# Performance work log

Hardware: AMD Instinct MI355X
Metric: run time of the kernel (lower is better)

The kernel has to match this reference:

```python
import jax, jax.numpy as jnp
import numpy as np

NUM_EXPERTS = 8
TOP_K = 2
D = 512
F = 2048
B, L = 4, 1024


def setup_inputs() -> dict:
    key = jax.random.key(0)
    ks = jax.random.split(key, 5)
    std = D ** -0.5
    return {
        "x": jax.random.normal(ks[0], (B, L, D), jnp.float32),
        "gate_w": jax.random.normal(ks[1], (NUM_EXPERTS, D), jnp.float32) * std,
        "w1": jax.random.normal(ks[2], (NUM_EXPERTS, F, D), jnp.float32) * std,
        "w2": jax.random.normal(ks[3], (NUM_EXPERTS, D, F), jnp.float32) * (F ** -0.5),
        "w3": jax.random.normal(ks[4], (NUM_EXPERTS, F, D), jnp.float32) * std,
    }


def reference(x, gate_w, w1, w2, w3):
    b, l, d = x.shape
    xf = x.reshape(-1, d)                      # [T, D]
    T = xf.shape[0]
    router_logits = xf @ gate_w.T              # [T, E]
    # top-k routing in float32 (as in original), softmax over selected logits
    topk_w, topk_idx = jax.lax.top_k(router_logits.astype(jnp.float32), TOP_K)
    topk_w = jax.nn.softmax(topk_w, axis=-1).astype(x.dtype)  # [T, K]
    # combine weights per (token, expert): scatter top-k weights into dense [T, E]
    cw = jnp.zeros((T, NUM_EXPERTS), x.dtype)
    cw = cw.at[jnp.arange(T)[:, None], topk_idx].add(topk_w)
    # per-expert gated FFN (SiLU(x w1^T) * (x w3^T)) w2^T, batched over experts
    h = jax.nn.silu(jnp.einsum('td,efd->etf', xf, w1)) * jnp.einsum('td,efd->etf', xf, w3)
    y = jnp.einsum('etf,edf->etd', h, w2)      # [E, T, D]
    out = jnp.einsum('te,etd->td', cw, y)      # weighted combine
    return out.reshape(b, l, d), router_logits
```

## Files before the change

### kernel.cpp

```cpp
#include <hip/hip_runtime.h>

#define TTOK 4096
#define NEXP 8
#define DDIM 512
#define FDIM 2048

typedef __attribute__((ext_vector_type(8))) short short8;
typedef __attribute__((ext_vector_type(4))) float floatx4;

__device__ __forceinline__ ushort f2b(float f) {
  unsigned u = __float_as_uint(f);
  u += 0x7fffu + ((u >> 16) & 1u);
  return (ushort)(u >> 16);
}

__device__ __forceinline__ void load16(void* lds, const void* g) {
  __builtin_amdgcn_global_load_lds(
      (const __attribute__((address_space(1))) unsigned int*)g,
      (__attribute__((address_space(3))) unsigned int*)lds, 16, 0, 0);
}

__global__ __launch_bounds__(256) void k_cvt3(
    const float* __restrict__ s1, ushort* __restrict__ d1,
    const float* __restrict__ s2, ushort* __restrict__ d2,
    const float* __restrict__ s3, ushort* __restrict__ d3, int n4)
{
  int i = blockIdx.x * 256 + threadIdx.x;
  const float* s; ushort* d; int j;
  if (i < n4)            { s = s1; d = d1; j = i; }
  else if (i < 2 * n4)   { s = s2; d = d2; j = i - n4; }
  else                   { s = s3; d = d3; j = i - 2 * n4; }
  float4 v = ((const float4*)s)[j];
  ushort4 b = { f2b(v.x), f2b(v.y), f2b(v.z), f2b(v.w) };
  ((ushort4*)d)[j] = b;
}

__global__ __launch_bounds__(256) void k_logits(
    const float* __restrict__ x, const float* __restrict__ gw,
    float* __restrict__ logits, int* __restrict__ tok_e,
    float2* __restrict__ tok_w, ushort* __restrict__ xb)
{
  const int lane = threadIdx.x & 63;
  const int t = blockIdx.x * 4 + (threadIdx.x >> 6);
  float xv[8];
#pragma unroll
  for (int i = 0; i < 8; ++i) xv[i] = x[(size_t)t * DDIM + lane + 64 * i];
#pragma unroll
  for (int i = 0; i < 8; ++i) xb[(size_t)t * DDIM + lane + 64 * i] = f2b(xv[i]);
  float lg[8];
#pragma unroll
  for (int e = 0; e < 8; ++e) {
    float a = 0.f;
#pragma unroll
    for (int i = 0; i < 8; ++i) a += xv[i] * gw[e * DDIM + lane + 64 * i];
#pragma unroll
    for (int s = 32; s; s >>= 1) a += __shfl_xor(a, s, 64);
    lg[e] = a;
  }
  if (lane < 8) logits[(size_t)t * 8 + lane] = lg[lane];
  if (lane == 0) {
    int i0 = 0; float v0 = lg[0];
#pragma unroll
    for (int e = 1; e < 8; ++e) { if (lg[e] > v0) { v0 = lg[e]; i0 = e; } }
    int i1 = -1; float v1 = -3.4e38f;
#pragma unroll
    for (int e = 0; e < 8; ++e) { if (e != i0 && lg[e] > v1) { v1 = lg[e]; i1 = e; } }
    float ex = expf(v1 - v0);
    float inv = 1.f / (1.f + ex);
    tok_e[t] = i0 | (i1 << 4);
    tok_w[t] = make_float2(inv, ex * inv);
  }
}

__global__ __launch_bounds__(256) void k_build(
    const int* __restrict__ tok_e, const float2* __restrict__ tok_w,
    int* __restrict__ counts, int* __restrict__ lists, float* __restrict__ wts)
{
  const int e = blockIdx.x;
  const int tid = threadIdx.x;
  const int lane = tid & 63, wid = tid >> 6;
  __shared__ int wcnt[4];
  __shared__ int sbase;
  if (tid == 0) sbase = 0;
  __syncthreads();

  for (int c = 0; c < TTOK; c += 256) {
    int t = c + tid;
    int pe = tok_e[t];
    bool m0 = (pe & 15) == e;
    bool m1 = ((pe >> 4) & 15) == e;
    bool m = m0 || m1;
    unsigned long long b = __ballot(m);
    int lpre = __popcll(b & ((1ull << lane) - 1ull));
    if (lane == 0) wcnt[wid] = __popcll(b);
    __syncthreads();
    int woff = 0;
#pragma unroll
    for (int i = 0; i < 4; ++i) if (i < wid) woff += wcnt[i];
    if (m) {
      float2 w = tok_w[t];
      int pos = sbase + woff + lpre;
      lists[e * TTOK + pos] = t;
      wts[e * TTOK + pos] = m0 ? w.x : w.y;
    }
    __syncthreads();
    if (tid == 0) sbase += wcnt[0] + wcnt[1] + wcnt[2] + wcnt[3];
    __syncthreads();
  }
  if (tid == 0) counts[e] = sbase;
}

__global__ void k_offsets(const int* __restrict__ counts, int* __restrict__ offs) {
  if (threadIdx.x == 0 && blockIdx.x == 0) {
    int s = 0;
    for (int e = 0; e < NEXP; ++e) { offs[e] = s; s += counts[e]; }
  }
}

__global__ __launch_bounds__(512) void k_ffn1(
    const ushort* __restrict__ xb, const ushort* __restrict__ w1b,
    const ushort* __restrict__ w3b, const int* __restrict__ counts,
    const int* __restrict__ offs, const int* __restrict__ lists,
    ushort* __restrict__ H)
{
  const int bid = blockIdx.x;
  const int widx = (bid & 7) * 512 + (bid >> 3);
  const int mt = widx & 31, e = (widx >> 5) & 7, f0t = widx >> 8;
  const int ne = counts[e];
  const int m0 = mt * 128;
  if (m0 >= ne) return;
  const int f0 = f0t * 128;
  const int tid = threadIdx.x;

  __shared__ ushort xs[2][128][32];
  __shared__ ushort w1s[2][128][32];
  __shared__ ushort w3s[2][128][32];
  __shared__ int toks[128];

  if (tid < 128) {
    int p = m0 + tid;
    toks[tid] = (p < ne) ? lists[e * TTOK + p] : 0;
  }
  __syncthreads();

  const int wid = tid >> 6, lane = tid & 63;
  const int wm = wid >> 2, wn = wid & 3;
  const int lr = lane & 15, lgp = lane >> 4;

  const int sr = tid >> 2, sc = (tid & 3) << 3;
  const ushort* xS  = xb + (size_t)toks[sr] * DDIM + sc;
  const ushort* w1S = w1b + (size_t)e * FDIM * DDIM + (size_t)(f0 + sr) * DDIM + sc;
  const ushort* w3S = w3b + (size_t)e * FDIM * DDIM + (size_t)(f0 + sr) * DDIM + sc;

#define FFN1_STAGE(B)                                                      \
  {                                                                        \
    load16((char*)&xs[B][0][0] + wid * 1024, xS);                          \
    load16((char*)&w1s[B][0][0] + wid * 1024, w1S);                        \
    load16((char*)&w3s[B][0][0] + wid * 1024, w3S);                        \
    xS += 32; w1S += 32; w3S += 32;                                        \
  }

#define FFN1_COMPUTE(B)                                                    \
  {                                                                        \
    short8 af[4], f1[2], f3[2];                                            \
    _Pragma("unroll")                                                      \
    for (int mf = 0; mf < 4; ++mf)                                         \
      af[mf] = *(const short8*)&xs[B][wm * 64 + mf * 16 + lr][lgp * 8];    \
    _Pragma("unroll")                                                      \
    for (int nf = 0; nf < 2; ++nf) {                                       \
      f1[nf] = *(const short8*)&w1s[B][wn * 32 + nf * 16 + lr][lgp * 8];   \
      f3[nf] = *(const short8*)&w3s[B][wn * 32 + nf * 16 + lr][lgp * 8];   \
    }                                                                      \
    _Pragma("unroll")                                                      \
    for (int mf = 0; mf < 4; ++mf)                                         \
      _Pragma("unroll")                                                    \
      for (int nf = 0; nf < 2; ++nf) {                                     \
        acc1[mf][nf] = __builtin_amdgcn_mfma_f32_16x16x32_bf16(            \
            af[mf], f1[nf], acc1[mf][nf], 0, 0, 0);                        \
        acc3[mf][nf] = __builtin_amdgcn_mfma_f32_16x16x32_bf16(            \
            af[mf], f3[nf], acc3[mf][nf], 0, 0, 0);                        \
      }                                                                    \
  }

  floatx4 acc1[4][2], acc3[4][2];
#pragma unroll
  for (int a = 0; a < 4; ++a)
#pragma unroll
    for (int b = 0; b < 2; ++b) { acc1[a][b] = (floatx4)0.f; acc3[a][b] = (floatx4)0.f; }

  FFN1_STAGE(0);
  __syncthreads();

  for (int t = 0; t < 16; t += 2) {
    if (t + 1 < 16) FFN1_STAGE(1);
    FFN1_COMPUTE(0);
    __syncthreads();
    if (t + 2 < 16) FFN1_STAGE(0);
    FFN1_COMPUTE(1);
    __syncthreads();
  }

  const int hb = offs[e];
#pragma unroll
  for (int mf = 0; mf < 4; ++mf) {
#pragma unroll
    for (int j = 0; j < 4; ++j) {
      int rloc = wm * 64 + mf * 16 + lgp * 4 + j;
      int p = m0 + rloc;
      if (p < ne) {
#pragma unroll
        for (int nf = 0; nf < 2; ++nf) {
          float h1 = acc1[mf][nf][j];
          float h3 = acc3[mf][nf][j];
          float sig = 1.f / (1.f + __expf(-h1));
          int f = f0 + wn * 32 + nf * 16 + lr;
          H[(size_t)(hb + p) * FDIM + f] = f2b(h1 * sig * h3);
        }
      }
    }
  }
#undef FFN1_STAGE
#undef FFN1_COMPUTE
}

__global__ __launch_bounds__(512) void k_ffn2(
    const ushort* __restrict__ w2b, const int* __restrict__ counts,
    const int* __restrict__ offs, const int* __restrict__ lists,
    const float* __restrict__ wts, const ushort* __restrict__ H,
    float* __restrict__ out)
{
  const int bid = blockIdx.x;
  const int widx = (bid & 7) * 128 + (bid >> 3);
  const int mt = widx & 31, e = (widx >> 5) & 7, d0t = widx >> 8;
  const int ne = counts[e];
  const int m0 = mt * 128;
  if (m0 >= ne) return;
  const int d0 = d0t * 128;
  const int tid = threadIdx.x;

  __shared__ ushort hs[2][2][128][32];
  __shared__ ushort w2s[2][2][128][32];
  __shared__ int toks[128];
  __shared__ float twt[128];

  const int hb = offs[e];
  if (tid < 128) {
    int p = m0 + tid;
    bool v = p < ne;
    toks[tid] = v ? lists[e * TTOK + p] : 0;
    twt[tid] = v ? wts[e * TTOK + p] : 0.f;
  }

  const int wid = tid >> 6, lane = tid & 63;
  const int wm = wid >> 2, wn = wid & 3;
  const int lr = lane & 15, lgp = lane >> 4;

  const int sr = tid >> 2, sc = (tid & 3) << 3;
  const int p0 = m0 + sr;
  const int hr = (p0 < ne) ? (hb + p0) : hb;
  const ushort* hS  = H + (size_t)hr * FDIM + sc;
  const ushort* w2S = w2b + (size_t)e * DDIM * FDIM + (size_t)(d0 + sr) * FDIM + sc;

#define FFN2_STAGE(B)                                                      \
  {                                                                        \
    load16((char*)&hs[B][0][0][0] + wid * 1024, hS);                       \
    load16((char*)&hs[B][1][0][0] + wid * 1024, hS + 32);                  \
    load16((char*)&w2s[B][0][0][0] + wid * 1024, w2S);                     \
    load16((char*)&w2s[B][1][0][0] + wid * 1024, w2S + 32);                \
    hS += 64; w2S += 64;                                                   \
  }

#define FFN2_COMPUTE(B)                                                    \
  {                                                                        \
    _Pragma("unroll")                                                      \
    for (int kk = 0; kk < 2; ++kk) {                                       \
      short8 af[4], bf[2];                                                 \
      _Pragma("unroll")                                                    \
      for (int mf = 0; mf < 4; ++mf)                                       \
        af[mf] = *(const short8*)&hs[B][kk][wm * 64 + mf * 16 + lr][lgp * 8]; \
      _Pragma("unroll")                                                    \
      for (int nf = 0; nf < 2; ++nf)                                       \
        bf[nf] = *(const short8*)&w2s[B][kk][wn * 32 + nf * 16 + lr][lgp * 8]; \
      _Pragma("unroll")                                                    \
      for (int mf = 0; mf < 4; ++mf)                                       \
        _Pragma("unroll")                                                  \
        for (int nf = 0; nf < 2; ++nf)                                     \
          acc[mf][nf] = __builtin_amdgcn_mfma_f32_16x16x32_bf16(           \
              af[mf], bf[nf], acc[mf][nf], 0, 0, 0);                       \
    }                                                                      \
  }

  floatx4 acc[4][2];
#pragma unroll
  for (int a = 0; a < 4; ++a)
#pragma unroll
    for (int b = 0; b < 2; ++b) acc[a][b] = (floatx4)0.f;

  FFN2_STAGE(0);
  __syncthreads();

  for (int t = 0; t < 32; t += 2) {
    if (t + 1 < 32) FFN2_STAGE(1);
    FFN2_COMPUTE(0);
    __syncthreads();
    if (t + 2 < 32) FFN2_STAGE(0);
    FFN2_COMPUTE(1);
    __syncthreads();
  }

#pragma unroll
  for (int mf = 0; mf < 4; ++mf) {
#pragma unroll
    for (int j = 0; j < 4; ++j) {
      int rloc = wm * 64 + mf * 16 + lgp * 4 + j;
      int p = m0 + rloc;
      if (p < ne) {
        int t = toks[rloc];
        float w = twt[rloc];
#pragma unroll
        for (int nf = 0; nf < 2; ++nf) {
          int d = d0 + wn * 32 + nf * 16 + lr;
          atomicAdd(&out[(size_t)t * DDIM + d], w * acc[mf][nf][j]);
        }
      }
    }
  }
#undef FFN2_STAGE
#undef FFN2_COMPUTE
}

extern "C" void kernel_launch(void* const* d_in, const int* in_sizes, int n_in,
                              void* d_out, int out_size, void* d_ws, size_t ws_size,
                              hipStream_t stream) {
  const float* x  = (const float*)d_in[0];
  const float* gw = (const float*)d_in[1];
  const float* w1 = (const float*)d_in[2];
  const float* w2 = (const float*)d_in[3];
  const float* w3 = (const float*)d_in[4];
  float* out = (float*)d_out;
  float* logits = out + (size_t)TTOK * DDIM;

  int* counts = (int*)d_ws;
  int* offs   = counts + 8;
  int* tok_e  = offs + 8;
  float2* tok_w = (float2*)(tok_e + TTOK);
  int* lists  = (int*)(tok_w + TTOK);
  float* wts  = (float*)(lists + NEXP * TTOK);
  ushort* xbb = (ushort*)(wts + NEXP * TTOK);
  ushort* w1b = xbb + (size_t)TTOK * DDIM;
  ushort* w3b = w1b + (size_t)NEXP * FDIM * DDIM;
  ushort* w2b = w3b + (size_t)NEXP * FDIM * DDIM;
  ushort* H   = w2b + (size_t)NEXP * DDIM * FDIM;

  hipMemsetAsync(d_out, 0, (size_t)TTOK * DDIM * sizeof(float), stream);

  const int nW = NEXP * FDIM * DDIM / 4;
  k_logits<<<TTOK / 4, 256, 0, stream>>>(x, gw, logits, tok_e, tok_w, xbb);
  k_build<<<NEXP, 256, 0, stream>>>(tok_e, tok_w, counts, lists, wts);
  k_offsets<<<1, 64, 0, stream>>>(counts, offs);

  k_cvt3<<<3 * nW / 256, 256, 0, stream>>>(w1, w1b, w3, w3b, w2, w2b, nW);

  k_ffn1<<<4096, 512, 0, stream>>>(xbb, w1b, w3b, counts, offs, lists, H);
  k_ffn2<<<1024, 512, 0, stream>>>(w2b, counts, offs, lists, wts, H, out);
}
```

Before: 160.5 us.

## Pre-tile operands into MFMA fragment layout and switch to 32x32x16 MFMA

Weights are converted to bf16 directly into a tiled layout that matches the MFMA fragments, and tokens are gathered into a padded, tiled per-expert X buffer. Both FFN kernels now use 256-thread blocks with 32x32x16 bf16 MFMAs and read LDS contiguously per lane, which removes the strided row loads and LDS bank conflicts. H is written in the same tiled layout so FFN2 can stream it directly. This adds a separate gather pass and a transposing conversion kernel, and it shrinks the per-block thread count, which may affect latency hiding.

Result: slower. 221.2 us (+37.8%).

```diff
diff --git a/kernel.cpp b/kernel.cpp
--- a/kernel.cpp
+++ b/kernel.cpp
@@ -4,9 +4,10 @@
 #define NEXP 8
 #define DDIM 512
 #define FDIM 2048
+#define HROWS 8576
 
 typedef __attribute__((ext_vector_type(8))) short short8;
-typedef __attribute__((ext_vector_type(4))) float floatx4;
+typedef __attribute__((ext_vector_type(16))) float floatx16;
 
 __device__ __forceinline__ ushort f2b(float f) {
   unsigned u = __float_as_uint(f);
@@ -20,33 +21,17 @@
       (__attribute__((address_space(3))) unsigned int*)lds, 16, 0, 0);
 }
 
-__global__ __launch_bounds__(256) void k_cvt3(
-    const float* __restrict__ s1, ushort* __restrict__ d1,
-    const float* __restrict__ s2, ushort* __restrict__ d2,
-    const float* __restrict__ s3, ushort* __restrict__ d3, int n4)
-{
-  int i = blockIdx.x * 256 + threadIdx.x;
-  const float* s; ushort* d; int j;
-  if (i < n4)            { s = s1; d = d1; j = i; }
-  else if (i < 2 * n4)   { s = s2; d = d2; j = i - n4; }
-  else                   { s = s3; d = d3; j = i - 2 * n4; }
-  float4 v = ((const float4*)s)[j];
-  ushort4 b = { f2b(v.x), f2b(v.y), f2b(v.z), f2b(v.w) };
-  ((ushort4*)d)[j] = b;
-}
 
 __global__ __launch_bounds__(256) void k_logits(
     const float* __restrict__ x, const float* __restrict__ gw,
     float* __restrict__ logits, int* __restrict__ tok_e,
-    float2* __restrict__ tok_w, ushort* __restrict__ xb)
+    float2* __restrict__ tok_w)
 {
   const int lane = threadIdx.x & 63;
   const int t = blockIdx.x * 4 + (threadIdx.x >> 6);
   float xv[8];
 #pragma unroll
   for (int i = 0; i < 8; ++i) xv[i] = x[(size_t)t * DDIM + lane + 64 * i];
-#pragma unroll
-  for (int i = 0; i < 8; ++i) xb[(size_t)t * DDIM + lane + 64 * i] = f2b(xv[i]);
   float lg[8];
 #pragma unroll
   for (int e = 0; e < 8; ++e) {
@@ -110,83 +95,131 @@
   if (tid == 0) counts[e] = sbase;
 }
 
-__global__ void k_offsets(const int* __restrict__ counts, int* __restrict__ offs) {
+__global__ void k_offsets(const int* __restrict__ counts, int* __restrict__ hbp) {
   if (threadIdx.x == 0 && blockIdx.x == 0) {
-    int s = 0;
-    for (int e = 0; e < NEXP; ++e) { offs[e] = s; s += counts[e]; }
-  }
-}
-
-__global__ __launch_bounds__(512) void k_ffn1(
-    const ushort* __restrict__ xb, const ushort* __restrict__ w1b,
-    const ushort* __restrict__ w3b, const int* __restrict__ counts,
-    const int* __restrict__ offs, const int* __restrict__ lists,
-    ushort* __restrict__ H)
+    int s = 0; hbp[0] = 0;
+    for (int e = 0; e < NEXP; ++e) { s += (counts[e] + 31) & ~31; hbp[e + 1] = s; }
+  }
+}
+
+__global__ __launch_bounds__(256) void k_gather(
+    const float* __restrict__ x, const int* __restrict__ counts,
+    const int* __restrict__ hbp, const int* __restrict__ lists,
+    ushort* __restrict__ Xg)
+{
+  int gid = blockIdx.x * 256 + threadIdx.x;
+  int gr = gid >> 6, dg = gid & 63;
+  if (gr >= hbp[8]) return;
+  int e = 0;
+  while (e < 7 && gr >= hbp[e + 1]) ++e;
+  int p = gr - hbp[e];
+  size_t dst = ((size_t)(gr >> 5) * 32 + (dg >> 1)) * 512 + (dg & 1) * 256 + (gr & 31) * 8;
+  short8 o = (short8)0;
+  if (p < counts[e]) {
+    int t = lists[e * TTOK + p];
+    const float* s = x + (size_t)t * DDIM + dg * 8;
+    float4 a = *(const float4*)s;
+    float4 b = *(const float4*)(s + 4);
+    o[0] = f2b(a.x); o[1] = f2b(a.y); o[2] = f2b(a.z); o[3] = f2b(a.w);
+    o[4] = f2b(b.x); o[5] = f2b(b.y); o[6] = f2b(b.z); o[7] = f2b(b.w);
+  }
+  *(short8*)&Xg[dst] = o;
+}
+
+__global__ __launch_bounds__(256) void k_cvtT(
+    const float* __restrict__ src, ushort* __restrict__ dst, int C, int cbShift)
+{
+  __shared__ ushort sm[4096];
+  const int bid = blockIdx.x, tid = threadIdx.x;
+  const int r0 = (bid >> cbShift) * 32;
+  const int c0 = (bid & ((1 << cbShift) - 1)) * 128;
+  const int KT = C >> 4;
+#pragma unroll
+  for (int i = 0; i < 4; ++i) {
+    int j = i * 1024 + tid * 4;
+    int lr = j >> 7, lc = j & 127;
+    float4 v = *(const float4*)&src[(size_t)(r0 + lr) * C + c0 + lc];
+    ushort4 b = { f2b(v.x), f2b(v.y), f2b(v.z), f2b(v.w) };
+    *(ushort4*)&sm[(lc >> 4) * 512 + (((lc >> 3) & 1) * 32 + lr) * 8 + (lc & 7)] = b;
+  }
+  __syncthreads();
+  size_t tb = ((size_t)(r0 >> 5) * KT + (c0 >> 4)) * 512;
+#pragma unroll
+  for (int i = 0; i < 2; ++i) {
+    int s = i * 256 + tid;
+    *(short8*)&dst[tb + s * 8] = *(const short8*)&sm[s * 8];
+  }
+}
+
+__global__ __launch_bounds__(256) void k_ffn1(
+    const ushort* __restrict__ Xg, const ushort* __restrict__ w1t,
+    const ushort* __restrict__ w3t, const int* __restrict__ counts,
+    const int* __restrict__ hbp, ushort* __restrict__ H)
 {
   const int bid = blockIdx.x;
   const int widx = (bid & 7) * 512 + (bid >> 3);
-  const int mt = widx & 31, e = (widx >> 5) & 7, f0t = widx >> 8;
+  const int mt = widx & 31, e = (widx >> 5) & 7, ft = widx >> 8;
   const int ne = counts[e];
   const int m0 = mt * 128;
   if (m0 >= ne) return;
-  const int f0 = f0t * 128;
+  const int f0 = ft * 128;
+  const int hb = hbp[e];
   const int tid = threadIdx.x;
-
-  __shared__ ushort xs[2][128][32];
-  __shared__ ushort w1s[2][128][32];
-  __shared__ ushort w3s[2][128][32];
-  __shared__ int toks[128];
-
-  if (tid < 128) {
-    int p = m0 + tid;
-    toks[tid] = (p < ne) ? lists[e * TTOK + p] : 0;
-  }
-  __syncthreads();
-
   const int wid = tid >> 6, lane = tid & 63;
-  const int wm = wid >> 2, wn = wid & 3;
-  const int lr = lane & 15, lgp = lane >> 4;
-
-  const int sr = tid >> 2, sc = (tid & 3) << 3;
-  const ushort* xS  = xb + (size_t)toks[sr] * DDIM + sc;
-  const ushort* w1S = w1b + (size_t)e * FDIM * DDIM + (size_t)(f0 + sr) * DDIM + sc;
-  const ushort* w3S = w3b + (size_t)e * FDIM * DDIM + (size_t)(f0 + sr) * DDIM + sc;
-
-#define FFN1_STAGE(B)                                                      \
-  {                                                                        \
-    load16((char*)&xs[B][0][0] + wid * 1024, xS);                          \
-    load16((char*)&w1s[B][0][0] + wid * 1024, w1S);                        \
-    load16((char*)&w3s[B][0][0] + wid * 1024, w3S);                        \
-    xS += 32; w1S += 32; w3S += 32;                                        \
-  }
-
-#define FFN1_COMPUTE(B)                                                    \
-  {                                                                        \
-    short8 af[4], f1[2], f3[2];                                            \
-    _Pragma("unroll")                                                      \
-    for (int mf = 0; mf < 4; ++mf)                                         \
-      af[mf] = *(const short8*)&xs[B][wm * 64 + mf * 16 + lr][lgp * 8];    \
-    _Pragma("unroll")                                                      \
-    for (int nf = 0; nf < 2; ++nf) {                                       \
-      f1[nf] = *(const short8*)&w1s[B][wn * 32 + nf * 16 + lr][lgp * 8];   \
-      f3[nf] = *(const short8*)&w3s[B][wn * 32 + nf * 16 + lr][lgp * 8];   \
-    }                                                                      \
-    _Pragma("unroll")                                                      \
-    for (int mf = 0; mf < 4; ++mf)                                         \
-      _Pragma("unroll")                                                    \
-      for (int nf = 0; nf < 2; ++nf) {                                     \
-        acc1[mf][nf] = __builtin_amdgcn_mfma_f32_16x16x32_bf16(            \
-            af[mf], f1[nf], acc1[mf][nf], 0, 0, 0);                        \
-        acc3[mf][nf] = __builtin_amdgcn_mfma_f32_16x16x32_bf16(            \
-            af[mf], f3[nf], acc3[mf][nf], 0, 0, 0);                        \
-      }                                                                    \
-  }
-
-  floatx4 acc1[4][2], acc3[4][2];
-#pragma unroll
-  for (int a = 0; a < 4; ++a)
-#pragma unroll
-    for (int b = 0; b < 2; ++b) { acc1[a][b] = (floatx4)0.f; acc3[a][b] = (floatx4)0.f; }
+  const int wm = wid >> 1, wn = wid & 1;
+  const int col = lane & 31, hi = lane >> 5;
+
+  __shared__ ushort Xls[2][4096], W1ls[2][4096], W3ls[2][4096];
+
+  const int rtX = (hb + m0) >> 5;
+  const int rtW = e * 64 + (f0 >> 5);
+  const ushort* sx[2]; const ushort* s1[2]; const ushort* s3[2];
+#pragma unroll
+  for (int i = 0; i < 2; ++i) {
+    int s = i * 256 + tid;
+    int rt = s >> 7, ktl = (s >> 6) & 1, ls = s & 63;
+    sx[i] = Xg  + ((size_t)(rtX + rt) * 32 + ktl) * 512 + ls * 8;
+    s1[i] = w1t + ((size_t)(rtW + rt) * 32 + ktl) * 512 + ls * 8;
+    s3[i] = w3t + ((size_t)(rtW + rt) * 32 + ktl) * 512 + ls * 8;
+  }
+
+#define FFN1_STAGE(B)                                                       \
+  { char* dx = (char*)&Xls[B][0] + wid * 1024;                              \
+    char* d1 = (char*)&W1ls[B][0] + wid * 1024;                             \
+    char* d3 = (char*)&W3ls[B][0] + wid * 1024;                             \
+    load16(dx, sx[0]); load16(dx + 4096, sx[1]);                            \
+    load16(d1, s1[0]); load16(d1 + 4096, s1[1]);                            \
+    load16(d3, s3[0]); load16(d3 + 4096, s3[1]);                            \
+    sx[0] += 1024; sx[1] += 1024; s1[0] += 1024; s1[1] += 1024;             \
+    s3[0] += 1024; s3[1] += 1024; }
+
+#define FFN1_COMPUTE(B)                                                     \
+  { _Pragma("unroll")                                                       \
+    for (int kk = 0; kk < 2; ++kk) {                                        \
+      short8 af[2], b1[2], b3[2];                                           \
+      _Pragma("unroll")                                                     \
+      for (int mf = 0; mf < 2; ++mf)                                        \
+        af[mf] = *(const short8*)&Xls[B][((wm * 2 + mf) * 2 + kk) * 512 + lane * 8]; \
+      _Pragma("unroll")                                                     \
+      for (int nf = 0; nf < 2; ++nf) {                                      \
+        b1[nf] = *(const short8*)&W1ls[B][((wn * 2 + nf) * 2 + kk) * 512 + lane * 8]; \
+        b3[nf] = *(const short8*)&W3ls[B][((wn * 2 + nf) * 2 + kk) * 512 + lane * 8]; \
+      }                                                                     \
+      _Pragma("unroll")                                                     \
+      for (int mf = 0; mf < 2; ++mf)                                        \
+        _Pragma("unroll")                                                   \
+        for (int nf = 0; nf < 2; ++nf) {                                    \
+          acc1[mf][nf] = __builtin_amdgcn_mfma_f32_32x32x16_bf16(           \
+              af[mf], b1[nf], acc1[mf][nf], 0, 0, 0);                       \
+          acc3[mf][nf] = __builtin_amdgcn_mfma_f32_32x32x16_bf16(           \
+              af[mf], b3[nf], acc3[mf][nf], 0, 0, 0);                       \
+        } } }
+
+  floatx16 acc1[2][2], acc3[2][2];
+#pragma unroll
+  for (int a = 0; a < 2; ++a)
+#pragma unroll
+    for (int b = 0; b < 2; ++b) { acc1[a][b] = (floatx16)0.f; acc3[a][b] = (floatx16)0.f; }
 
   FFN1_STAGE(0);
   __syncthreads();
@@ -200,21 +233,24 @@
     __syncthreads();
   }
 
-  const int hb = offs[e];
-#pragma unroll
-  for (int mf = 0; mf < 4; ++mf) {
-#pragma unroll
-    for (int j = 0; j < 4; ++j) {
-      int rloc = wm * 64 + mf * 16 + lgp * 4 + j;
-      int p = m0 + rloc;
-      if (p < ne) {
-#pragma unroll
-        for (int nf = 0; nf < 2; ++nf) {
-          float h1 = acc1[mf][nf][j];
-          float h3 = acc3[mf][nf][j];
+#pragma unroll
+  for (int mf = 0; mf < 2; ++mf) {
+    const int rbase = wm * 64 + mf * 32;
+    const size_t rowTile = (size_t)rtX + wm * 2 + mf;
+#pragma unroll
+    for (int nf = 0; nf < 2; ++nf) {
+      const int fbase = f0 + wn * 64 + nf * 32;
+      size_t hbase = (rowTile * 128 + (fbase >> 4) + (col >> 4)) * 512
+                   + ((col >> 3) & 1) * 256 + (col & 7);
+      floatx16 v1 = acc1[mf][nf], v3 = acc3[mf][nf];
+#pragma unroll
+      for (int j = 0; j < 16; ++j) {
+        int ri = (j & 3) + 8 * (j >> 2) + 4 * hi;
+        int p = m0 + rbase + ri;
+        if (p < ne) {
+          float h1 = v1[j], h3 = v3[j];
           float sig = 1.f / (1.f + __expf(-h1));
-          int f = f0 + wn * 32 + nf * 16 + lr;
-          H[(size_t)(hb + p) * FDIM + f] = f2b(h1 * sig * h3);
+          H[hbase + (size_t)ri * 8] = f2b(h1 * sig * h3);
         }
       }
     }
@@ -223,27 +259,29 @@
 #undef FFN1_COMPUTE
 }
 
-__global__ __launch_bounds__(512) void k_ffn2(
-    const ushort* __restrict__ w2b, const int* __restrict__ counts,
-    const int* __restrict__ offs, const int* __restrict__ lists,
-    const float* __restrict__ wts, const ushort* __restrict__ H,
+__global__ __launch_bounds__(256) void k_ffn2(
+    const ushort* __restrict__ Ht, const ushort* __restrict__ w2t,
+    const int* __restrict__ counts, const int* __restrict__ hbp,
+    const int* __restrict__ lists, const float* __restrict__ wts,
     float* __restrict__ out)
 {
   const int bid = blockIdx.x;
   const int widx = (bid & 7) * 128 + (bid >> 3);
-  const int mt = widx & 31, e = (widx >> 5) & 7, d0t = widx >> 8;
+  const int mt = widx & 31, e = (widx >> 5) & 7, dt = widx >> 8;
   const int ne = counts[e];
   const int m0 = mt * 128;
   if (m0 >= ne) return;
-  const int d0 = d0t * 128;
+  const int d0 = dt * 128;
+  const int hb = hbp[e];
   const int tid = threadIdx.x;
-
-  __shared__ ushort hs[2][2][128][32];
-  __shared__ ushort w2s[2][2][128][32];
+  const int wid = tid >> 6, lane = tid & 63;
+  const int wm = wid >> 1, wn = wid & 1;
+  const int col = lane & 31, hi = lane >> 5;
+
+  __shared__ ushort Hls[2][4096], W2ls[2][4096];
   __shared__ int toks[128];
   __shared__ float twt[128];
 
-  const int hb = offs[e];
   if (tid < 128) {
     int p = m0 + tid;
     bool v = p < ne;
@@ -251,76 +289,74 @@
     twt[tid] = v ? wts[e * TTOK + p] : 0.f;
   }
 
-  const int wid = tid >> 6, lane = tid & 63;
-  const int wm = wid >> 2, wn = wid & 3;
-  const int lr = lane & 15, lgp = lane >> 4;
-
-  const int sr = tid >> 2, sc = (tid & 3) << 3;
-  const int p0 = m0 + sr;
-  const int hr = (p0 < ne) ? (hb + p0) : hb;
-  const ushort* hS  = H + (size_t)hr * FDIM + sc;
-  const ushort* w2S = w2b + (size_t)e * DDIM * FDIM + (size_t)(d0 + sr) * FDIM + sc;
+  const int rtH = (hb + m0) >> 5;
+  const int rtW = e * 16 + (d0 >> 5);
+  const ushort* sh[2]; const ushort* sw[2];
+#pragma unroll
+  for (int i = 0; i < 2; ++i) {
+    int s = i * 256 + tid;
+    int rt = s >> 7, ktl = (s >> 6) & 1, ls = s & 63;
+    sh[i] = Ht  + ((size_t)(rtH + rt) * 128 + ktl) * 512 + ls * 8;
+    sw[i] = w2t + ((size_t)(rtW + rt) * 128 + ktl) * 512 + ls * 8;
+  }
 
 #define FFN2_STAGE(B)                                                      \
-  {                                                                        \
-    load16((char*)&hs[B][0][0][0] + wid * 1024, hS);                       \
-    load16((char*)&hs[B][1][0][0] + wid * 1024, hS + 32);                  \
-    load16((char*)&w2s[B][0][0][0] + wid * 1024, w2S);                     \
-    load16((char*)&w2s[B][1][0][0] + wid * 1024, w2S + 32);                \
-    hS += 64; w2S += 64;                                                   \
-  }
+  { char* dh = (char*)&Hls[B][0] + wid * 1024;                             \
+    char* dw = (char*)&W2ls[B][0] + wid * 1024;                            \
+    load16(dh, sh[0]); load16(dh + 4096, sh[1]);                           \
+    load16(dw, sw[0]); load16(dw + 4096, sw[1]);                           \
+    sh[0] += 1024; sh[1] += 1024; sw[0] += 1024; sw[1] += 1024; }
 
 #define FFN2_COMPUTE(B)                                                    \
-  {                                                                        \
-    _Pragma("unroll")                                                      \
+  { _Pragma("unroll")                                                      \
     for (int kk = 0; kk < 2; ++kk) {                                       \
-      short8 af[4], bf[2];                                                 \
+      short8 af[2], bf[2];                                                 \
       _Pragma("unroll")                                                    \
-      for (int mf = 0; mf < 4; ++mf)                                       \
-        af[mf] = *(const short8*)&hs[B][kk][wm * 64 + mf * 16 + lr][lgp * 8]; \
+      for (int mf = 0; mf < 2; ++mf)                                       \
+        af[mf] = *(const short8*)&Hls[B][((wm * 2 + mf) * 2 + kk) * 512 + lane * 8]; \
       _Pragma("unroll")                                                    \
       for (int nf = 0; nf < 2; ++nf)                                       \
-        bf[nf] = *(const short8*)&w2s[B][kk][wn * 32 + nf * 16 + lr][lgp * 8]; \
+        bf[nf] = *(const short8*)&W2ls[B][((wn * 2 + nf) * 2 + kk) * 512 + lane * 8]; \
       _Pragma("unroll")                                                    \
-      for (int mf = 0; mf < 4; ++mf)                                       \
+      for (int mf = 0; mf < 2; ++mf)                                       \
         _Pragma("unroll")                                                  \
         for (int nf = 0; nf < 2; ++nf)                                     \
-          acc[mf][nf] = __builtin_amdgcn_mfma_f32_16x16x32_bf16(           \
+          acc[mf][nf] = __builtin_amdgcn_mfma_f32_32x32x16_bf16(           \
               af[mf], bf[nf], acc[mf][nf], 0, 0, 0);                       \
-    }                                                                      \
-  }
-
-  floatx4 acc[4][2];
-#pragma unroll
-  for (int a = 0; a < 4; ++a)
-#pragma unroll
-    for (int b = 0; b < 2; ++b) acc[a][b] = (floatx4)0.f;
+    } }
+
+  floatx16 acc[2][2];
+#pragma unroll
+  for (int a = 0; a < 2; ++a)
+#pragma unroll
+    for (int b = 0; b < 2; ++b) acc[a][b] = (floatx16)0.f;
 
   FFN2_STAGE(0);
   __syncthreads();
 
-  for (int t = 0; t < 32; t += 2) {
-    if (t + 1 < 32) FFN2_STAGE(1);
+  for (int t = 0; t < 64; t += 2) {
+    if (t + 1 < 64) FFN2_STAGE(1);
     FFN2_COMPUTE(0);
     __syncthreads();
-    if (t + 2 < 32) FFN2_STAGE(0);
+    if (t + 2 < 64) FFN2_STAGE(0);
     FFN2_COMPUTE(1);
     __syncthreads();
   }
 
 #pragma unroll
-  for (int mf = 0; mf < 4; ++mf) {
-#pragma unroll
-    for (int j = 0; j < 4; ++j) {
-      int rloc = wm * 64 + mf * 16 + lgp * 4 + j;
-      int p = m0 + rloc;
-      if (p < ne) {
-        int t = toks[rloc];
-        float w = twt[rloc];
-#pragma unroll
-        for (int nf = 0; nf < 2; ++nf) {
-          int d = d0 + wn * 32 + nf * 16 + lr;
-          atomicAdd(&out[(size_t)t * DDIM + d], w * acc[mf][nf][j]);
+  for (int mf = 0; mf < 2; ++mf) {
+    const int rbase = wm * 64 + mf * 32;
+#pragma unroll
+    for (int nf = 0; nf < 2; ++nf) {
+      const int d = d0 + wn * 64 + nf * 32 + col;
+      floatx16 v = acc[mf][nf];
+#pragma unroll
+      for (int j = 0; j < 16; ++j) {
+        int ri = (j & 3) + 8 * (j >> 2) + 4 * hi;
+        int rloc = rbase + ri;
+        int p = m0 + rloc;
+        if (p < ne) {
+          atomicAdd(&out[(size_t)toks[rloc] * DDIM + d], twt[rloc] * v[j]);
         }
       }
     }
@@ -341,26 +377,28 @@
   float* logits = out + (size_t)TTOK * DDIM;
 
   int* counts = (int*)d_ws;
-  int* offs   = counts + 8;
-  int* tok_e  = offs + 8;
+  int* hbp    = counts + 8;
+  int* tok_e  = hbp + 16;
   float2* tok_w = (float2*)(tok_e + TTOK);
   int* lists  = (int*)(tok_w + TTOK);
   float* wts  = (float*)(lists + NEXP * TTOK);
-  ushort* xbb = (ushort*)(wts + NEXP * TTOK);
-  ushort* w1b = xbb + (size_t)TTOK * DDIM;
-  ushort* w3b = w1b + (size_t)NEXP * FDIM * DDIM;
-  ushort* w2b = w3b + (size_t)NEXP * FDIM * DDIM;
-  ushort* H   = w2b + (size_t)NEXP * DDIM * FDIM;
+  ushort* w1t = (ushort*)(wts + NEXP * TTOK);
+  ushort* w3t = w1t + (size_t)NEXP * FDIM * DDIM;
+  ushort* w2t = w3t + (size_t)NEXP * FDIM * DDIM;
+  ushort* Xg  = w2t + (size_t)NEXP * DDIM * FDIM;
+  ushort* H   = Xg + (size_t)HROWS * DDIM;
 
   hipMemsetAsync(d_out, 0, (size_t)TTOK * DDIM * sizeof(float), stream);
 
-  const int nW = NEXP * FDIM * DDIM / 4;
-  k_logits<<<TTOK / 4, 256, 0, stream>>>(x, gw, logits, tok_e, tok_w, xbb);
+  k_logits<<<TTOK / 4, 256, 0, stream>>>(x, gw, logits, tok_e, tok_w);
   k_build<<<NEXP, 256, 0, stream>>>(tok_e, tok_w, counts, lists, wts);
-  k_offsets<<<1, 64, 0, stream>>>(counts, offs);
-
-  k_cvt3<<<3 * nW / 256, 256, 0, stream>>>(w1, w1b, w3, w3b, w2, w2b, nW);
-
-  k_ffn1<<<4096, 512, 0, stream>>>(xbb, w1b, w3b, counts, offs, lists, H);
-  k_ffn2<<<1024, 512, 0, stream>>>(w2b, counts, offs, lists, wts, H, out);
-}
+  k_offsets<<<1, 64, 0, stream>>>(counts, hbp);
+  k_gather<<<(8448 * 64) / 256, 256, 0, stream>>>(x, counts, hbp, lists, Xg);
+
+  k_cvtT<<<2048, 256, 0, stream>>>(w1, w1t, 512, 2);
+  k_cvtT<<<2048, 256, 0, stream>>>(w3, w3t, 512, 2);
+  k_cvtT<<<2048, 256, 0, stream>>>(w2, w2t, 2048, 4);
+
+  k_ffn1<<<4096, 256, 0, stream>>>(Xg, w1t, w3t, counts, hbp, H);
+  k_ffn2<<<1024, 256, 0, stream>>>(H, w2t, counts, hbp, lists, wts, out);
+}
```
